# Kernel optimization log

Hardware: AMD Instinct MI355X
Metric: run time of the kernel (lower is better)

## Reference

```python
import jax, jax.numpy as jnp
import numpy as np

N_NODES = 50000
N_EDGES = 600000
IN_F = 128
HID = 128
OUT = 128
CLS = 128
N_GRAPHS = 64
LN_EPS = 1e-5


def _ln(h, g, b):
    m = jnp.mean(h, axis=-1, keepdims=True)
    v = jnp.var(h, axis=-1, keepdims=True)
    return (h - m) * jax.lax.rsqrt(v + LN_EPS) * g + b


def _segment_softmax(logits, seg, num_segments):
    m = jax.ops.segment_max(logits, seg, num_segments=num_segments)
    e = jnp.exp(logits - m[seg])
    s = jax.ops.segment_sum(e, seg, num_segments=num_segments)
    return e / s[seg]


def _gat_conv(x, src, dst, aux, w_lin, b_lin, aw1, ab1, lng, lnb, aw2, ab2):
    xl = x @ w_lin + b_lin                      # [N, out]
    sf = xl[src]                                # [E, out]
    df = xl[dst]                                # [E, out]
    ef = jnp.concatenate([sf, df, aux], axis=-1)  # [E, 2*out+2]
    h = jax.nn.relu(_ln(ef @ aw1 + ab1, lng, lnb))
    logits = h @ aw2 + ab2                      # [E, 1]
    att = _segment_softmax(logits, dst, xl.shape[0])
    num = jax.ops.segment_sum(sf * att, dst, num_segments=xl.shape[0])
    cnt = jax.ops.segment_sum(jnp.ones((src.shape[0], 1), xl.dtype), dst, num_segments=xl.shape[0])
    out = num / jnp.maximum(cnt, 1.0)           # scatter_mean (empty rows -> 0)
    return out + xl


def setup_inputs() -> dict:
    key = jax.random.key(0)
    ks = jax.random.split(key, 24)
    s = 0.05
    d = {
        'x': jax.random.normal(ks[0], (N_NODES, IN_F), jnp.float32),
        'edge_index': jax.random.randint(ks[1], (2, N_EDGES), 0, N_NODES, jnp.int64),
        'aux_info': jax.random.normal(ks[2], (N_EDGES, 2), jnp.float32),
        'batch': jnp.sort(jax.random.randint(ks[3], (N_NODES,), 0, N_GRAPHS, jnp.int64)),
        # conv1 params (in->hid)
        'w_lin1': jax.random.normal(ks[4], (IN_F, HID), jnp.float32) * s,
        'b_lin1': jnp.zeros((HID,), jnp.float32),
        'aw1_1': jax.random.normal(ks[5], (2 * HID + 2, HID), jnp.float32) * s,
        'ab1_1': jnp.zeros((HID,), jnp.float32),
        'lng1': jnp.ones((HID,), jnp.float32),
        'lnb1': jnp.zeros((HID,), jnp.float32),
        'aw2_1': jax.random.normal(ks[6], (HID, 1), jnp.float32) * s,
        'ab2_1': jnp.zeros((1,), jnp.float32),
        # conv2 params (hid->out)
        'w_lin2': jax.random.normal(ks[7], (HID, OUT), jnp.float32) * s,
        'b_lin2': jnp.zeros((OUT,), jnp.float32),
        'aw1_2': jax.random.normal(ks[8], (2 * OUT + 2, HID), jnp.float32) * s,
        'ab1_2': jnp.zeros((HID,), jnp.float32),
        'lng2': jnp.ones((HID,), jnp.float32),
        'lnb2': jnp.zeros((HID,), jnp.float32),
        'aw2_2': jax.random.normal(ks[9], (HID, 1), jnp.float32) * s,
        'ab2_2': jnp.zeros((1,), jnp.float32),
        # head
        'cls_w': jax.random.normal(ks[10], (OUT, CLS), jnp.float32) * s,
        'cls_b': jnp.zeros((CLS,), jnp.float32),
        'norm_g': jnp.ones((OUT,), jnp.float32),
        'norm_b': jnp.zeros((OUT,), jnp.float32),
    }
    return d


def reference(x, edge_index, aux_info, batch,
              w_lin1, b_lin1, aw1_1, ab1_1, lng1, lnb1, aw2_1, ab2_1,
              w_lin2, b_lin2, aw1_2, ab1_2, lng2, lnb2, aw2_2, ab2_2,
              cls_w, cls_b, norm_g, norm_b):
    src, dst = edge_index[0], edge_index[1]
    h = _gat_conv(x, src, dst, aux_info, w_lin1, b_lin1, aw1_1, ab1_1, lng1, lnb1, aw2_1, ab2_1)
    h = jax.nn.relu(h)
    h = _gat_conv(h, src, dst, aux_info, w_lin2, b_lin2, aw1_2, ab1_2, lng2, lnb2, aw2_2, ab2_2)
    h = _ln(h, norm_g, norm_b)                  # [N, out]
    fusion = jax.ops.segment_max(h, batch, num_segments=N_GRAPHS)  # global max pool
    cls = fusion @ cls_w + cls_b                # [G, cls]
    return (h, cls)
```

## Files before the change

kernel.cpp:

```cpp
#include <hip/hip_runtime.h>
#include <math.h>

typedef __attribute__((ext_vector_type(8))) short short8v;
typedef __attribute__((ext_vector_type(4))) float f32x4;
typedef __attribute__((ext_vector_type(2))) float f32x2;

__device__ __forceinline__ unsigned short f2bf(float f) {
    union { float f; unsigned int u; } v; v.f = f;
    unsigned int r = v.u + 0x7FFFu + ((v.u >> 16) & 1u);
    return (unsigned short)(r >> 16);
}
__device__ __forceinline__ float bflo(unsigned int v) {
    union { unsigned int u; float f; } x; x.u = v << 16; return x.f;
}
__device__ __forceinline__ float bfhi(unsigned int v) {
    union { unsigned int u; float f; } x; x.u = v & 0xFFFF0000u; return x.f;
}
__device__ __forceinline__ unsigned char f2fp8(float f) {
    return (unsigned char)(__builtin_amdgcn_cvt_pk_fp8_f32(f, f, 0, false) & 0xFF);
}
__device__ __forceinline__ unsigned pkrtz(float a, float b) {
    unsigned d;
    asm("v_cvt_pkrtz_f16_f32 %0, %1, %2" : "=v"(d) : "v"(a), "v"(b));
    return d;
}
__device__ __forceinline__ float fdot2a(unsigned a, unsigned b, float c) {
    float d;
    asm("v_dot2_f32_f16 %0, %1, %2, %3" : "=v"(d) : "v"(a), "v"(b), "v"(c));
    return d;
}
__device__ __forceinline__ unsigned pk_fma_f16(unsigned a, unsigned b, unsigned c) {
    unsigned d;
    asm("v_pk_fma_f16 %0, %1, %2, %3" : "=v"(d) : "v"(a), "v"(b), "v"(c));
    return d;
}
__device__ __forceinline__ unsigned pk_max0_f16(unsigned a, unsigned z) {
    unsigned d;
    asm("v_pk_max_f16 %0, %1, %2" : "=v"(d) : "v"(a), "v"(z));
    return d;
}

__global__ void hist_kernel(const int* __restrict__ dst, int* __restrict__ deg, int E) {
    int e = blockIdx.x * 256 + threadIdx.x;
    if (e < E) atomicAdd(&deg[dst[e]], 1);
}

__global__ __launch_bounds__(256) void scan1_kernel(const int* __restrict__ deg,
                                                    int* __restrict__ rp,
                                                    int* __restrict__ bsum, int N) {
    const int lane = threadIdx.x & 63, wid = threadIdx.x >> 6;
    int i = blockIdx.x * 256 + threadIdx.x;
    int v = (i < N) ? deg[i] : 0;
    int val = v;
#pragma unroll
    for (int off = 1; off < 64; off <<= 1) {
        int t = __shfl_up(val, off, 64);
        if (lane >= off) val += t;
    }
    __shared__ int ws[4];
    if (lane == 63) ws[wid] = val;
    __syncthreads();
    int pre = 0;
#pragma unroll
    for (int w = 0; w < 4; ++w) pre += (w < wid) ? ws[w] : 0;
    int incl = pre + val;
    if (i < N) rp[i] = incl - v;
    if (threadIdx.x == 255) bsum[blockIdx.x] = incl;
}

__global__ __launch_bounds__(256) void scan2_kernel(int* __restrict__ bsum, int NB) {
    const int lane = threadIdx.x & 63, wid = threadIdx.x >> 6;
    int t = threadIdx.x;
    int v = (t < NB) ? bsum[t] : 0;
    int val = v;
#pragma unroll
    for (int off = 1; off < 64; off <<= 1) {
        int t2 = __shfl_up(val, off, 64);
        if (lane >= off) val += t2;
    }
    __shared__ int ws[4];
    if (lane == 63) ws[wid] = val;
    __syncthreads();
    int pre = 0;
#pragma unroll
    for (int w = 0; w < 4; ++w) pre += (w < wid) ? ws[w] : 0;
    int excl = pre + val - v;
    __syncthreads();
    if (t < NB) bsum[t] = excl;
}

__global__ __launch_bounds__(256) void scan3_kernel(int* __restrict__ rp,
                                                    const int* __restrict__ bsum,
                                                    int N, int E) {
    int i = blockIdx.x * 256 + threadIdx.x;
    if (i < N) rp[i] += bsum[blockIdx.x];
    if (i == 0) rp[N] = E;
}

__global__ void scatter_kernel(const int* __restrict__ src, const int* __restrict__ dst,
                               const float* __restrict__ aux,
                               const int* __restrict__ rowptr, int* __restrict__ cursor,
                               uint2* __restrict__ er, int E) {
    int e = blockIdx.x * 256 + threadIdx.x;
    if (e < E) {
        int d = dst[e];
        int pos = rowptr[d] + atomicAdd(&cursor[d], 1);
        float2 a = *(const float2*)(aux + 2 * e);
        uint2 r;
        r.x = (unsigned)src[e] | ((unsigned)d << 16);
        r.y = (unsigned)f2bf(a.x) | ((unsigned)f2bf(a.y) << 16);
        er[pos] = r;
    }
}

__global__ void bounds_kernel(const int* __restrict__ batch, int* __restrict__ gstart,
                              int* __restrict__ gend, int N) {
    int i = blockIdx.x * 256 + threadIdx.x;
    if (i >= N) return;
    int b = batch[i];
    if (i == 0 || batch[i - 1] != b) gstart[b] = i;
    if (i == N - 1 || batch[i + 1] != b) gend[b] = i + 1;
}

__global__ __launch_bounds__(256) void pack6_kernel(const float* __restrict__ s0,
                                                    const float* __restrict__ s1,
                                                    const float* __restrict__ s2,
                                                    const float* __restrict__ s3,
                                                    const float* __restrict__ s4,
                                                    const float* __restrict__ s5,
                                                    unsigned short* __restrict__ Wp) {
    int which = blockIdx.x >> 6;
    const float* W = (which == 0) ? s0 : (which == 1) ? s1 : (which == 2) ? s2
                   : (which == 3) ? s3 : (which == 4) ? s4 : s5;
    int t = (blockIdx.x & 63) * 256 + threadIdx.x;
    int j = t & 7, l = (t >> 3) & 63, ct = (t >> 9) & 7, ks = t >> 12;
    int k = ks * 32 + (l >> 4) * 8 + j;
    int n = ct * 16 + (l & 15);
    Wp[which * 16384 + t] = f2bf(W[k * 128 + n]);
}

template <int ABF>
__global__ __launch_bounds__(256) void linpq_kernel(const void* __restrict__ Av,
                                                    const unsigned short* __restrict__ WpL,
                                                    const float* __restrict__ bias,
                                                    const unsigned short* __restrict__ WpP,
                                                    const unsigned short* __restrict__ WpQ,
                                                    const float* __restrict__ ab1,
                                                    unsigned short* __restrict__ Dbf,
                                                    unsigned char* __restrict__ Vf8,
                                                    unsigned char* __restrict__ Pf8,
                                                    unsigned char* __restrict__ Qf8, int M) {
    __shared__ unsigned short lds[32][136];
    __shared__ unsigned char ldsV[32][128];
    __shared__ unsigned char ldsP[32][128];
    __shared__ unsigned char ldsQ[32][128];
    const int l = threadIdx.x & 63, w = threadIdx.x >> 6;
    const int tile = w >> 1, ch = w & 1;
    const int rowb = blockIdx.x * 32;
    const int rowbase = rowb + tile * 16;
    const int r = rowbase + (l & 15);
    const int kc = (l >> 4) * 8;

    short8v afr[4];
    if (r < M) {
        if (ABF) {
            const unsigned short* ap = (const unsigned short*)Av + (size_t)r * 128 + kc;
#pragma unroll
            for (int ks = 0; ks < 4; ++ks)
                afr[ks] = *(const short8v*)(ap + ks * 32);
        } else {
            const float* ap = (const float*)Av + (size_t)r * 128 + kc;
#pragma unroll
            for (int ks = 0; ks < 4; ++ks) {
                float4 x0 = *(const float4*)(ap + ks * 32);
                float4 x1 = *(const float4*)(ap + ks * 32 + 4);
                unsigned short u[8] = {f2bf(x0.x), f2bf(x0.y), f2bf(x0.z), f2bf(x0.w),
                                       f2bf(x1.x), f2bf(x1.y), f2bf(x1.z), f2bf(x1.w)};
                afr[ks] = *(short8v*)u;
            }
        }
    } else {
#pragma unroll
        for (int ks = 0; ks < 4; ++ks)
#pragma unroll
            for (int j = 0; j < 8; ++j) afr[ks][j] = 0;
    }

    f32x4 acc[4];
#pragma unroll
    for (int c = 0; c < 4; ++c)
#pragma unroll
        for (int j = 0; j < 4; ++j) acc[c][j] = 0.f;

    const short8v* wl = (const short8v*)WpL;
#pragma unroll
    for (int ks = 0; ks < 4; ++ks)
#pragma unroll
        for (int c = 0; c < 4; ++c)
            acc[c] = __builtin_amdgcn_mfma_f32_16x16x32_bf16(
                afr[ks], wl[(ks * 8 + ch * 4 + c) * 64 + l], acc[c], 0, 0, 0);

    const int lrb = tile * 16 + (l >> 4) * 4;
#pragma unroll
    for (int c = 0; c < 4; ++c) {
        int col = (ch * 4 + c) * 16 + (l & 15);
        float bv = bias ? bias[col] : 0.f;
#pragma unroll
        for (int j = 0; j < 4; ++j) {
            float v = acc[c][j] + bv;
            lds[lrb + j][col] = f2bf(v);
            ldsV[lrb + j][col] = f2fp8(v);
        }
    }
    __syncthreads();

    {
        int r2 = threadIdx.x >> 3, q2 = threadIdx.x & 7;
        if (rowb + r2 < M) {
            *(uint4*)(Dbf + (size_t)(rowb + r2) * 128 + q2 * 16) =
                *(uint4*)&lds[r2][q2 * 16];
            *(uint4*)(Dbf + (size_t)(rowb + r2) * 128 + q2 * 16 + 8) =
                *(uint4*)&lds[r2][q2 * 16 + 8];
            *(uint4*)(Vf8 + (size_t)(rowb + r2) * 128 + q2 * 16) =
                *(uint4*)&ldsV[r2][q2 * 16];
        }
    }

    short8v xfr[4];
#pragma unroll
    for (int ks = 0; ks < 4; ++ks)
        xfr[ks] = *(const short8v*)&lds[tile * 16 + (l & 15)][kc + ks * 32];

    f32x4 accP[4], accQ[4];
#pragma unroll
    for (int c = 0; c < 4; ++c)
#pragma unroll
        for (int j = 0; j < 4; ++j) { accP[c][j] = 0.f; accQ[c][j] = 0.f; }

    const short8v* wp = (const short8v*)WpP;
    const short8v* wq = (const short8v*)WpQ;
#pragma unroll
    for (int ks = 0; ks < 4; ++ks)
#pragma unroll
        for (int c = 0; c < 4; ++c) {
            accP[c] = __builtin_amdgcn_mfma_f32_16x16x32_bf16(
                xfr[ks], wp[(ks * 8 + ch * 4 + c) * 64 + l], accP[c], 0, 0, 0);
            accQ[c] = __builtin_amdgcn_mfma_f32_16x16x32_bf16(
                xfr[ks], wq[(ks * 8 + ch * 4 + c) * 64 + l], accQ[c], 0, 0, 0);
        }

#pragma unroll
    for (int c = 0; c < 4; ++c) {
        int col = (ch * 4 + c) * 16 + (l & 15);
        float b1v = ab1[col];
#pragma unroll
        for (int j = 0; j < 4; ++j) {
            ldsP[lrb + j][col] = f2fp8(accP[c][j]);
            ldsQ[lrb + j][col] = f2fp8(accQ[c][j] + b1v);
        }
    }
    __syncthreads();
    {
        int r2 = threadIdx.x >> 3, q2 = threadIdx.x & 7;
        if (rowb + r2 < M) {
            *(uint4*)(Pf8 + (size_t)(rowb + r2) * 128 + q2 * 16) =
                *(uint4*)&ldsP[r2][q2 * 16];
            *(uint4*)(Qf8 + (size_t)(rowb + r2) * 128 + q2 * 16) =
                *(uint4*)&ldsQ[r2][q2 * 16];
        }
    }
}

__global__ __launch_bounds__(256, 4) void attn_edge_kernel(
    const unsigned char* __restrict__ Pf8, const unsigned char* __restrict__ Qf8,
    const uint2* __restrict__ er,
    const float* __restrict__ wa0, const float* __restrict__ wa1,
    const float* __restrict__ lng, const float* __restrict__ lnb,
    const float* __restrict__ aw2, const float* __restrict__ ab2,
    float* __restrict__ wt, int E) {
    __shared__ float lwf[256];
    __shared__ unsigned lwh[192];
    {
        int idx = threadIdx.x;
        int arr = idx >> 7, rem = idx & 127;
        int par = rem >> 6, c = (rem >> 2) & 15, e = rem & 3;
        const float* sp = arr ? wa1 : wa0;
        lwf[(((arr * 16 + c) << 1) + par) * 4 + e] = sp[rem];
        if (idx < 192) {
            int a2 = idx >> 6, rem2 = idx & 63;
            int p2 = rem2 >> 5;
            int c2 = (rem2 >> 1) & 15;
            int pr = rem2 & 1;
            int chn = p2 * 64 + c2 * 4 + pr * 2;
            const float* s2 = (a2 == 0) ? lng : (a2 == 1) ? lnb : aw2;
            lwh[(((a2 * 16 + c2) << 1) + p2) * 2 + pr] = pkrtz(s2[chn], s2[chn + 1]);
        }
    }
    __syncthreads();
    const int slot = blockIdx.x * 128 + ((int)threadIdx.x >> 1);
    if (slot >= E) return;
    const int par = threadIdx.x & 1;
    const unsigned one2 = 0x3C003C00u;
    const unsigned zero2 = 0u;
    const int co = par << 6;

    uint2 ev = er[slot];
    const int sn = (int)(ev.x & 0xFFFFu);
    const int dn = (int)(ev.x >> 16);
    const float ax = bflo(ev.y), ay = bfhi(ev.y);

    const uint4* prow = (const uint4*)(Pf8 + (size_t)sn * 128 + co);
    const uint4* qrow = (const uint4*)(Qf8 + (size_t)dn * 128 + co);

    float r1 = 0.f, r2 = 0.f;
    unsigned tp[32];

#pragma unroll
    for (int g = 0; g < 4; ++g) {
        uint4 pv = prow[g];
        uint4 qv = qrow[g];
        unsigned pwa[4] = {pv.x, pv.y, pv.z, pv.w};
        unsigned qwa[4] = {qv.x, qv.y, qv.z, qv.w};
#pragma unroll
        for (int cc = 0; cc < 4; ++cc) {
            const int c = g * 4 + cc;
            f32x2 plo = __builtin_amdgcn_cvt_pk_f32_fp8((int)pwa[cc], false);
            f32x2 phi = __builtin_amdgcn_cvt_pk_f32_fp8((int)pwa[cc], true);
            f32x2 qlo = __builtin_amdgcn_cvt_pk_f32_fp8((int)qwa[cc], false);
            f32x2 qhi = __builtin_amdgcn_cvt_pk_f32_fp8((int)qwa[cc], true);
            float4 w0v = *(const float4*)&lwf[((c << 1) + par) * 4];
            float4 w1v = *(const float4*)&lwf[(((16 + c) << 1) + par) * 4];
            float t0 = plo[0] + qlo[0] + ax * w0v.x + ay * w1v.x;
            float t1 = plo[1] + qlo[1] + ax * w0v.y + ay * w1v.y;
            float t2 = phi[0] + qhi[0] + ax * w0v.z + ay * w1v.z;
            float t3 = phi[1] + qhi[1] + ax * w0v.w + ay * w1v.w;
            unsigned p0 = pkrtz(t0, t1);
            unsigned p1 = pkrtz(t2, t3);
            tp[2 * c] = p0;
            tp[2 * c + 1] = p1;
            r1 = fdot2a(p0, one2, r1);
            r1 = fdot2a(p1, one2, r1);
            r2 = fdot2a(p0, p0, r2);
            r2 = fdot2a(p1, p1, r2);
        }
    }
    r1 += __shfl_xor(r1, 1, 64);
    r2 += __shfl_xor(r2, 1, 64);
    float mean = r1 * (1.f / 128.f);
    float rstd = rsqrtf(r2 * (1.f / 128.f) - mean * mean + 1e-5f);
    float mr = mean * rstd;
    unsigned rstd2 = pkrtz(rstd, rstd);
    unsigned nmr2 = pkrtz(-mr, -mr);

    float dot = 0.f;
#pragma unroll
    for (int c = 0; c < 16; ++c) {
        unsigned base = (unsigned)(((c << 1) + par) * 2);
        uint2 gg = *(const uint2*)&lwh[base];
        uint2 ll = *(const uint2*)&lwh[64 + base];
        uint2 ww = *(const uint2*)&lwh[128 + base];
        unsigned u0 = pk_fma_f16(tp[2 * c], rstd2, nmr2);
        u0 = pk_fma_f16(u0, gg.x, ll.x);
        u0 = pk_max0_f16(u0, zero2);
        dot = fdot2a(u0, ww.x, dot);
        unsigned u1 = pk_fma_f16(tp[2 * c + 1], rstd2, nmr2);
        u1 = pk_fma_f16(u1, gg.y, ll.y);
        u1 = pk_max0_f16(u1, zero2);
        dot = fdot2a(u1, ww.y, dot);
    }
    dot += __shfl_xor(dot, 1, 64);
    if (par == 0) wt[slot] = __expf(dot + ab2[0]);
}

template <int MODE>
__global__ __launch_bounds__(256) void aggr_kernel(
    const unsigned short* __restrict__ xlbf, const unsigned char* __restrict__ Vf8,
    const float* __restrict__ wt,
    const uint2* __restrict__ er, const int* __restrict__ rowptr,
    const float* __restrict__ g, const float* __restrict__ b,
    void* __restrict__ out, int N) {
    const int lane8 = threadIdx.x & 7;
    const int v = blockIdx.x * 32 + ((int)threadIdx.x >> 3);
    if (v >= N) return;
    const int jb = lane8 * 16;

    const int s0 = rowptr[v], s1e = rowptr[v + 1];
    const int deg = s1e - s0;
    float acc[16];
#pragma unroll
    for (int k = 0; k < 16; ++k) acc[k] = 0.f;
    float wsum = 0.f;

    uint4 v0 = make_uint4(0, 0, 0, 0), v1 = v0;
    float wb0 = 0.f, wb1 = 0.f;
#define GATH2(idx, VV, WW)                                                       \
    if ((idx) < s1e) {                                                           \
        int sn_ = (int)(er[idx].x & 0xFFFFu);                                    \
        VV = *(const uint4*)(Vf8 + (size_t)sn_ * 128 + jb);                      \
        WW = wt[idx];                                                            \
    }
    GATH2(s0, v0, wb0)
    GATH2(s0 + 1, v1, wb1)

    for (int i = s0; i < s1e; i += 2) {
        uint4 c0 = v0, c1 = v1;
        float u0 = wb0;
        float u1 = (i + 1 < s1e) ? wb1 : 0.f;
        GATH2(i + 2, v0, wb0)
        GATH2(i + 3, v1, wb1)
        wsum += u0 + u1;
        unsigned d0[4] = {c0.x, c0.y, c0.z, c0.w};
        unsigned d1[4] = {c1.x, c1.y, c1.z, c1.w};
#pragma unroll
        for (int k = 0; k < 4; ++k) {
            f32x2 alo = __builtin_amdgcn_cvt_pk_f32_fp8((int)d0[k], false);
            f32x2 ahi = __builtin_amdgcn_cvt_pk_f32_fp8((int)d0[k], true);
            f32x2 blo = __builtin_amdgcn_cvt_pk_f32_fp8((int)d1[k], false);
            f32x2 bhi = __builtin_amdgcn_cvt_pk_f32_fp8((int)d1[k], true);
            acc[4 * k + 0] += u0 * alo[0] + u1 * blo[0];
            acc[4 * k + 1] += u0 * alo[1] + u1 * blo[1];
            acc[4 * k + 2] += u0 * ahi[0] + u1 * bhi[0];
            acc[4 * k + 3] += u0 * ahi[1] + u1 * bhi[1];
        }
    }
#undef GATH2

    const float ns = (deg > 0) ? 1.f / (wsum * (float)deg) : 0.f;
    float o[16];
    const unsigned short* xp = xlbf + (size_t)v * 128 + jb;
    uint4 xa = *(const uint4*)xp;
    uint4 xb = *(const uint4*)(xp + 8);
    unsigned xw[8] = {xa.x, xa.y, xa.z, xa.w, xb.x, xb.y, xb.z, xb.w};
#pragma unroll
    for (int k = 0; k < 8; ++k) {
        o[2 * k] = bflo(xw[k]) + acc[2 * k] * ns;
        o[2 * k + 1] = bfhi(xw[k]) + acc[2 * k + 1] * ns;
    }

    if (MODE == 0) {
        unsigned short* op = (unsigned short*)out + (size_t)v * 128 + jb;
        unsigned opk[8];
#pragma unroll
        for (int k = 0; k < 8; ++k)
            opk[k] = (unsigned)f2bf(fmaxf(o[2 * k], 0.f)) |
                     ((unsigned)f2bf(fmaxf(o[2 * k + 1], 0.f)) << 16);
        *(uint4*)op = make_uint4(opk[0], opk[1], opk[2], opk[3]);
        *(uint4*)(op + 8) = make_uint4(opk[4], opk[5], opk[6], opk[7]);
    } else {
        float r1 = 0.f, r2 = 0.f;
#pragma unroll
        for (int k = 0; k < 16; ++k) { r1 += o[k]; r2 = fmaf(o[k], o[k], r2); }
#pragma unroll
        for (int mk = 4; mk >= 1; mk >>= 1) {
            r1 += __shfl_xor(r1, mk, 64);
            r2 += __shfl_xor(r2, mk, 64);
        }
        float mean = r1 * (1.f / 128.f);
        float rstd = rsqrtf(r2 * (1.f / 128.f) - mean * mean + 1e-5f);
        float mr = mean * rstd;
        float* op = (float*)out + (size_t)v * 128 + jb;
#pragma unroll
        for (int k4 = 0; k4 < 4; ++k4) {
            float4 gv = *(const float4*)(g + jb + 4 * k4);
            float4 bv = *(const float4*)(b + jb + 4 * k4);
            float4 r;
            r.x = fmaf(fmaf(o[4 * k4 + 0], rstd, -mr), gv.x, bv.x);
            r.y = fmaf(fmaf(o[4 * k4 + 1], rstd, -mr), gv.y, bv.y);
            r.z = fmaf(fmaf(o[4 * k4 + 2], rstd, -mr), gv.z, bv.z);
            r.w = fmaf(fmaf(o[4 * k4 + 3], rstd, -mr), gv.w, bv.w);
            *(float4*)(op + 4 * k4) = r;
        }
    }
}

__global__ __launch_bounds__(128) void pool1_kernel(const float* __restrict__ h,
                                                    const int* __restrict__ gstart,
                                                    const int* __restrict__ gend,
                                                    float* __restrict__ part) {
    int gph = blockIdx.x >> 4;
    int sl = blockIdx.x & 15;
    int col = threadIdx.x;
    int s = gstart[gph], e = gend[gph];
    float m = -INFINITY;
    for (int r = s + sl; r < e; r += 16) m = fmaxf(m, h[(size_t)r * 128 + col]);
    part[(size_t)blockIdx.x * 128 + col] = m;
}

__global__ __launch_bounds__(128) void cls_kernel(const float* __restrict__ part,
                                                  const float* __restrict__ cw,
                                                  const float* __restrict__ cb,
                                                  float* __restrict__ out) {
    int gph = blockIdx.x, c = threadIdx.x;
    float m = -INFINITY;
#pragma unroll
    for (int sl = 0; sl < 16; ++sl) m = fmaxf(m, part[(size_t)(gph * 16 + sl) * 128 + c]);
    __shared__ float f[128];
    f[c] = m;
    __syncthreads();
    float acc = cb[c];
#pragma unroll 8
    for (int k = 0; k < 128; ++k) acc += f[k] * cw[k * 128 + c];
    out[gph * 128 + c] = acc;
}

extern "C" void kernel_launch(void* const* d_in, const int* in_sizes, int n_in,
                              void* d_out, int out_size, void* d_ws, size_t ws_size,
                              hipStream_t stream) {
    const float* x      = (const float*)d_in[0];
    const int*   ei     = (const int*)d_in[1];
    const float* aux    = (const float*)d_in[2];
    const int*   batch  = (const int*)d_in[3];
    const float* w_lin1 = (const float*)d_in[4];
    const float* b_lin1 = (const float*)d_in[5];
    const float* aw1_1  = (const float*)d_in[6];
    const float* ab1_1  = (const float*)d_in[7];
    const float* lng1   = (const float*)d_in[8];
    const float* lnb1   = (const float*)d_in[9];
    const float* aw2_1  = (const float*)d_in[10];
    const float* ab2_1  = (const float*)d_in[11];
    const float* w_lin2 = (const float*)d_in[12];
    const float* b_lin2 = (const float*)d_in[13];
    const float* aw1_2  = (const float*)d_in[14];
    const float* ab1_2  = (const float*)d_in[15];
    const float* lng2   = (const float*)d_in[16];
    const float* lnb2   = (const float*)d_in[17];
    const float* aw2_2  = (const float*)d_in[18];
    const float* ab2_2  = (const float*)d_in[19];
    const float* cls_w  = (const float*)d_in[20];
    const float* cls_b  = (const float*)d_in[21];
    const float* norm_g = (const float*)d_in[22];
    const float* norm_b = (const float*)d_in[23];

    const int N = in_sizes[0] / 128;
    const int E = in_sizes[2] / 2;
    const int G = 64;
    const int* src = ei;
    const int* dst = ei + E;

    char* wsp = (char*)d_ws;
    unsigned short* xlbf  = (unsigned short*)wsp;   wsp += (size_t)N * 128 * 2;
    unsigned short* h1bf  = (unsigned short*)wsp;   wsp += (size_t)N * 128 * 2;
    unsigned char*  Pf8   = (unsigned char*)wsp;    wsp += (size_t)N * 128;
    unsigned char*  Qf8   = (unsigned char*)wsp;    wsp += (size_t)N * 128;
    unsigned char*  Vf8   = (unsigned char*)wsp;    wsp += (size_t)N * 128;
    unsigned short* wpack = (unsigned short*)wsp;   wsp += 6 * 16384 * 2;
    float*          part  = (float*)wsp;            wsp += (size_t)1024 * 128 * 4;
    uint2*          er    = (uint2*)wsp;            wsp += (size_t)E * 8;
    float*          wt    = (float*)wsp;            wsp += (size_t)E * 4;
    int*            bsum    = (int*)wsp;            wsp += 256 * 4;
    int*            deg     = (int*)wsp;            wsp += (size_t)N * 4;
    int*            cursor  = (int*)wsp;            wsp += (size_t)N * 4;
    int*            rowptr  = (int*)wsp;            wsp += (size_t)(N + 1) * 4;
    int*            gstart  = (int*)wsp;            wsp += (size_t)G * 4;
    int*            gend    = (int*)wsp;            wsp += (size_t)G * 4;

    unsigned short* wp_lin1 = wpack;
    unsigned short* wp_s1   = wpack + 16384;
    unsigned short* wp_d1   = wpack + 2 * 16384;
    unsigned short* wp_lin2 = wpack + 3 * 16384;
    unsigned short* wp_s2   = wpack + 4 * 16384;
    unsigned short* wp_d2   = wpack + 5 * 16384;

    float* hout   = (float*)d_out;
    float* clsout = hout + (size_t)N * 128;

    hipMemsetAsync(deg, 0, (size_t)(2 * N) * sizeof(int), stream);
    hipMemsetAsync(gstart, 0, (size_t)(2 * G) * sizeof(int), stream);

    const int eb = (E + 255) / 256;
    const int nb = (N + 255) / 256;
    const int lb = (N + 31) / 32;
    const int atb = (E + 127) / 128;
    const int agb = (N + 31) / 32;

    hist_kernel<<<eb, 256, 0, stream>>>(dst, deg, E);
    scan1_kernel<<<nb, 256, 0, stream>>>(deg, rowptr, bsum, N);
    scan2_kernel<<<1, 256, 0, stream>>>(bsum, nb);
    scan3_kernel<<<nb, 256, 0, stream>>>(rowptr, bsum, N, E);
    scatter_kernel<<<eb, 256, 0, stream>>>(src, dst, aux, rowptr, cursor, er, E);
    bounds_kernel<<<nb, 256, 0, stream>>>(batch, gstart, gend, N);

    pack6_kernel<<<384, 256, 0, stream>>>(w_lin1, aw1_1, aw1_1 + 128 * 128,
                                          w_lin2, aw1_2, aw1_2 + 128 * 128, wpack);

    linpq_kernel<0><<<lb, 256, 0, stream>>>(x, wp_lin1, b_lin1, wp_s1, wp_d1, ab1_1,
                                            xlbf, Vf8, Pf8, Qf8, N);
    attn_edge_kernel<<<atb, 256, 0, stream>>>(Pf8, Qf8, er,
                                              aw1_1 + 256 * 128, aw1_1 + 257 * 128,
                                              lng1, lnb1, aw2_1, ab2_1, wt, E);
    aggr_kernel<0><<<agb, 256, 0, stream>>>(xlbf, Vf8, wt, er, rowptr,
                                            nullptr, nullptr, h1bf, N);
    linpq_kernel<1><<<lb, 256, 0, stream>>>(h1bf, wp_lin2, b_lin2, wp_s2, wp_d2, ab1_2,
                                            xlbf, Vf8, Pf8, Qf8, N);
    attn_edge_kernel<<<atb, 256, 0, stream>>>(Pf8, Qf8, er,
                                              aw1_2 + 256 * 128, aw1_2 + 257 * 128,
                                              lng2, lnb2, aw2_2, ab2_2, wt, E);
    aggr_kernel<1><<<agb, 256, 0, stream>>>(xlbf, Vf8, wt, er, rowptr,
                                            norm_g, norm_b, hout, N);
    pool1_kernel<<<G * 16, 128, 0, stream>>>(hout, gstart, gend, part);
    cls_kernel<<<G, 128, 0, stream>>>(part, cls_w, cls_b, clsout);
}
```

Baseline: 238.6 us.

## Precompose linear and attention weights to run all three GEMMs from input

Adds a small kernel that precomputes W_lin·W_s and W_lin·W_d (plus fused biases) for both convs, so the P and Q projections are computed directly from the input rows instead of from the rounded intermediate xl. The linpq kernel then issues all three MFMA chains from the same A fragments in one pass, removing the LDS reload of xl, a barrier and a second epilogue. The LDS rows for the fp8 tiles are padded to 144 bytes to reduce bank conflicts. The cost is an extra weight-fusion launch per call and slightly different rounding, since P and Q no longer pass through bf16 xl.

Result: slower. 248.3 us (+4.1%).

```diff
diff --git a/kernel.cpp b/kernel.cpp
--- a/kernel.cpp
+++ b/kernel.cpp
@@ -120,6 +120,33 @@
     int b = batch[i];
     if (i == 0 || batch[i - 1] != b) gstart[b] = i;
     if (i == N - 1 || batch[i + 1] != b) gend[b] = i + 1;
+}
+
+__global__ __launch_bounds__(128) void fuse_kernel(
+    const float* __restrict__ wl1, const float* __restrict__ bl1,
+    const float* __restrict__ aw11, const float* __restrict__ ab11,
+    const float* __restrict__ wl2, const float* __restrict__ bl2,
+    const float* __restrict__ aw12, const float* __restrict__ ab12,
+    float* __restrict__ fst) {
+    int blk = blockIdx.x;
+    int mat = blk / 129;
+    int k = blk % 129;
+    int n = threadIdx.x;
+    int conv = mat >> 1, which = mat & 1;
+    const float* WL = conv ? wl2 : wl1;
+    const float* BL = conv ? bl2 : bl1;
+    const float* AW = conv ? aw12 : aw11;
+    const float* AB = conv ? ab12 : ab11;
+    const float* WS = AW + which * 128 * 128;
+    float acc = 0.f;
+    if (k < 128) {
+        for (int m = 0; m < 128; ++m) acc = fmaf(WL[k * 128 + m], WS[m * 128 + n], acc);
+        fst[(size_t)mat * 129 * 128 + k * 128 + n] = acc;
+    } else {
+        for (int m = 0; m < 128; ++m) acc = fmaf(BL[m], WS[m * 128 + n], acc);
+        if (which == 1) acc += AB[n];
+        fst[(size_t)mat * 129 * 128 + 128 * 128 + n] = acc;
+    }
 }
 
 __global__ __launch_bounds__(256) void pack6_kernel(const float* __restrict__ s0,
@@ -145,15 +172,16 @@
                                                     const float* __restrict__ bias,
                                                     const unsigned short* __restrict__ WpP,
                                                     const unsigned short* __restrict__ WpQ,
-                                                    const float* __restrict__ ab1,
+                                                    const float* __restrict__ biasP,
+                                                    const float* __restrict__ biasQ,
                                                     unsigned short* __restrict__ Dbf,
                                                     unsigned char* __restrict__ Vf8,
                                                     unsigned char* __restrict__ Pf8,
                                                     unsigned char* __restrict__ Qf8, int M) {
     __shared__ unsigned short lds[32][136];
-    __shared__ unsigned char ldsV[32][128];
-    __shared__ unsigned char ldsP[32][128];
-    __shared__ unsigned char ldsQ[32][128];
+    __shared__ unsigned char ldsV[32][144];
+    __shared__ unsigned char ldsP[32][144];
+    __shared__ unsigned char ldsQ[32][144];
     const int l = threadIdx.x & 63, w = threadIdx.x >> 6;
     const int tile = w >> 1, ch = w & 1;
     const int rowb = blockIdx.x * 32;
@@ -186,30 +214,39 @@
             for (int j = 0; j < 8; ++j) afr[ks][j] = 0;
     }
 
-    f32x4 acc[4];
+    f32x4 acc[4], accP[4], accQ[4];
 #pragma unroll
     for (int c = 0; c < 4; ++c)
 #pragma unroll
-        for (int j = 0; j < 4; ++j) acc[c][j] = 0.f;
+        for (int j = 0; j < 4; ++j) { acc[c][j] = 0.f; accP[c][j] = 0.f; accQ[c][j] = 0.f; }
 
     const short8v* wl = (const short8v*)WpL;
+    const short8v* wp = (const short8v*)WpP;
+    const short8v* wq = (const short8v*)WpQ;
 #pragma unroll
     for (int ks = 0; ks < 4; ++ks)
 #pragma unroll
-        for (int c = 0; c < 4; ++c)
-            acc[c] = __builtin_amdgcn_mfma_f32_16x16x32_bf16(
-                afr[ks], wl[(ks * 8 + ch * 4 + c) * 64 + l], acc[c], 0, 0, 0);
+        for (int c = 0; c < 4; ++c) {
+            int fi = (ks * 8 + ch * 4 + c) * 64 + l;
+            acc[c] = __builtin_amdgcn_mfma_f32_16x16x32_bf16(afr[ks], wl[fi], acc[c], 0, 0, 0);
+            accP[c] = __builtin_amdgcn_mfma_f32_16x16x32_bf16(afr[ks], wp[fi], accP[c], 0, 0, 0);
+            accQ[c] = __builtin_amdgcn_mfma_f32_16x16x32_bf16(afr[ks], wq[fi], accQ[c], 0, 0, 0);
+        }
 
     const int lrb = tile * 16 + (l >> 4) * 4;
 #pragma unroll
     for (int c = 0; c < 4; ++c) {
         int col = (ch * 4 + c) * 16 + (l & 15);
         float bv = bias ? bias[col] : 0.f;
+        float bp = biasP[col];
+        float bq = biasQ[col];
 #pragma unroll
         for (int j = 0; j < 4; ++j) {
             float v = acc[c][j] + bv;
             lds[lrb + j][col] = f2bf(v);
             ldsV[lrb + j][col] = f2fp8(v);
+            ldsP[lrb + j][col] = f2fp8(accP[c][j] + bp);
+            ldsQ[lrb + j][col] = f2fp8(accQ[c][j] + bq);
         }
     }
     __syncthreads();
@@ -223,46 +260,6 @@
                 *(uint4*)&lds[r2][q2 * 16 + 8];
             *(uint4*)(Vf8 + (size_t)(rowb + r2) * 128 + q2 * 16) =
                 *(uint4*)&ldsV[r2][q2 * 16];
-        }
-    }
-
-    short8v xfr[4];
-#pragma unroll
-    for (int ks = 0; ks < 4; ++ks)
-        xfr[ks] = *(const short8v*)&lds[tile * 16 + (l & 15)][kc + ks * 32];
-
-    f32x4 accP[4], accQ[4];
-#pragma unroll
-    for (int c = 0; c < 4; ++c)
-#pragma unroll
-        for (int j = 0; j < 4; ++j) { accP[c][j] = 0.f; accQ[c][j] = 0.f; }
-
-    const short8v* wp = (const short8v*)WpP;
-    const short8v* wq = (const short8v*)WpQ;
-#pragma unroll
-    for (int ks = 0; ks < 4; ++ks)
-#pragma unroll
-        for (int c = 0; c < 4; ++c) {
-            accP[c] = __builtin_amdgcn_mfma_f32_16x16x32_bf16(
-                xfr[ks], wp[(ks * 8 + ch * 4 + c) * 64 + l], accP[c], 0, 0, 0);
-            accQ[c] = __builtin_amdgcn_mfma_f32_16x16x32_bf16(
-                xfr[ks], wq[(ks * 8 + ch * 4 + c) * 64 + l], accQ[c], 0, 0, 0);
-        }
-
-#pragma unroll
-    for (int c = 0; c < 4; ++c) {
-        int col = (ch * 4 + c) * 16 + (l & 15);
-        float b1v = ab1[col];
-#pragma unroll
-        for (int j = 0; j < 4; ++j) {
-            ldsP[lrb + j][col] = f2fp8(accP[c][j]);
-            ldsQ[lrb + j][col] = f2fp8(accQ[c][j] + b1v);
-        }
-    }
-    __syncthreads();
-    {
-        int r2 = threadIdx.x >> 3, q2 = threadIdx.x & 7;
-        if (rowb + r2 < M) {
             *(uint4*)(Pf8 + (size_t)(rowb + r2) * 128 + q2 * 16) =
                 *(uint4*)&ldsP[r2][q2 * 16];
             *(uint4*)(Qf8 + (size_t)(rowb + r2) * 128 + q2 * 16) =
@@ -544,6 +541,7 @@
     unsigned char*  Qf8   = (unsigned char*)wsp;    wsp += (size_t)N * 128;
     unsigned char*  Vf8   = (unsigned char*)wsp;    wsp += (size_t)N * 128;
     unsigned short* wpack = (unsigned short*)wsp;   wsp += 6 * 16384 * 2;
+    float*          fst   = (float*)wsp;            wsp += (size_t)4 * 129 * 128 * 4;
     float*          part  = (float*)wsp;            wsp += (size_t)1024 * 128 * 4;
     uint2*          er    = (uint2*)wsp;            wsp += (size_t)E * 8;
     float*          wt    = (float*)wsp;            wsp += (size_t)E * 4;
@@ -561,6 +559,15 @@
     unsigned short* wp_s2   = wpack + 4 * 16384;
     unsigned short* wp_d2   = wpack + 5 * 16384;
 
+    float* fP1 = fst + (size_t)0 * 129 * 128;
+    float* fQ1 = fst + (size_t)1 * 129 * 128;
+    float* fP2 = fst + (size_t)2 * 129 * 128;
+    float* fQ2 = fst + (size_t)3 * 129 * 128;
+    float* bP1 = fP1 + 128 * 128;
+    float* bQ1 = fQ1 + 128 * 128;
+    float* bP2 = fP2 + 128 * 128;
+    float* bQ2 = fQ2 + 128 * 128;
+
     float* hout   = (float*)d_out;
     float* clsout = hout + (size_t)N * 128;
 
@@ -580,18 +587,19 @@
     scatter_kernel<<<eb, 256, 0, stream>>>(src, dst, aux, rowptr, cursor, er, E);
     bounds_kernel<<<nb, 256, 0, stream>>>(batch, gstart, gend, N);
 
-    pack6_kernel<<<384, 256, 0, stream>>>(w_lin1, aw1_1, aw1_1 + 128 * 128,
-                                          w_lin2, aw1_2, aw1_2 + 128 * 128, wpack);
-
-    linpq_kernel<0><<<lb, 256, 0, stream>>>(x, wp_lin1, b_lin1, wp_s1, wp_d1, ab1_1,
-                                            xlbf, Vf8, Pf8, Qf8, N);
+    fuse_kernel<<<4 * 129, 128, 0, stream>>>(w_lin1, b_lin1, aw1_1, ab1_1,
+                                             w_lin2, b_lin2, aw1_2, ab1_2, fst);
+    pack6_kernel<<<384, 256, 0, stream>>>(w_lin1, fP1, fQ1, w_lin2, fP2, fQ2, wpack);
+
+    linpq_kernel<0><<<lb, 256, 0, stream>>>(x, wp_lin1, b_lin1, wp_s1, wp_d1,
+                                            bP1, bQ1, xlbf, Vf8, Pf8, Qf8, N);
     attn_edge_kernel<<<atb, 256, 0, stream>>>(Pf8, Qf8, er,
                                               aw1_1 + 256 * 128, aw1_1 + 257 * 128,
                                               lng1, lnb1, aw2_1, ab2_1, wt, E);
     aggr_kernel<0><<<agb, 256, 0, stream>>>(xlbf, Vf8, wt, er, rowptr,
                                             nullptr, nullptr, h1bf, N);
-    linpq_kernel<1><<<lb, 256, 0, stream>>>(h1bf, wp_lin2, b_lin2, wp_s2, wp_d2, ab1_2,
-                                            xlbf, Vf8, Pf8, Qf8, N);
+    linpq_kernel<1><<<lb, 256, 0, stream>>>(h1bf, wp_lin2, b_lin2, wp_s2, wp_d2,
+                                            bP2, bQ2, xlbf, Vf8, Pf8, Qf8, N);
     attn_edge_kernel<<<atb, 256, 0, stream>>>(Pf8, Qf8, er,
                                               aw1_2 + 256 * 128, aw1_2 + 257 * 128,
                                               lng2, lnb2, aw2_2, ab2_2, wt, E);
```
